# Kernel tuning notes

Hardware: AMD Instinct MI355X
Metric: run time of the kernel (lower is better)

The kernel has to match this reference:

```python
import jax, jax.numpy as jnp
import numpy as np

# --- fake-quant helpers (Brevitas-style simulated int4 with STE) ---

def _fq(x, scale, qmin, qmax):
    # fake quantize with straight-through estimator
    q = jnp.clip(jnp.round(x / scale), qmin, qmax) * scale
    return x + jax.lax.stop_gradient(q - x)

def quant_act_signed4(x):
    # signed 4-bit symmetric activation quant: scale = max|x| / 7
    scale = jax.lax.stop_gradient(jnp.maximum(jnp.max(jnp.abs(x)), 1e-8) / 7.0)
    return _fq(x, scale, -8, 7), scale

def quant_relu4(x):
    # QuantReLU: relu then unsigned 4-bit quant, scale = max / 15
    x = jax.nn.relu(x)
    scale = jax.lax.stop_gradient(jnp.maximum(jnp.max(x), 1e-8) / 15.0)
    return _fq(x, scale, 0, 15), scale

def quant_w4(w):
    # per-tensor symmetric 4-bit weight quant
    scale = jax.lax.stop_gradient(jnp.maximum(jnp.max(jnp.abs(w)), 1e-8) / 7.0)
    return _fq(w, scale, -8, 7), scale

def quant_bias32(b, in_scale, w_scale):
    # Int32Bias: bias quantized at scale = input_scale * weight_scale
    s = in_scale * w_scale
    return _fq(b, s, -(2.0**31), 2.0**31 - 1.0)

def conv2d(x, w, b):
    y = jax.lax.conv_general_dilated(x, w, (1, 1), 'VALID',
                                     dimension_numbers=('NCHW', 'OIHW', 'NCHW'))
    return y + b[None, :, None, None]


def setup_inputs() -> dict:
    key = jax.random.key(0)
    ks = jax.random.split(key, 9)
    f32 = jnp.float32
    return {
        'x':   jax.random.normal(ks[0], (32, 3, 224, 224), f32),
        'w1':  jax.random.normal(ks[1], (32, 3, 3, 3), f32) * 0.1,
        'b1':  jax.random.normal(ks[2], (32,), f32) * 0.05,
        'w2':  jax.random.normal(ks[3], (64, 32, 3, 3), f32) * 0.06,
        'b2':  jax.random.normal(ks[4], (64,), f32) * 0.05,
        'wf1': jax.random.normal(ks[5], (128, 64), f32) * 0.1,
        'bf1': jax.random.normal(ks[6], (128,), f32) * 0.05,
        'wf2': jax.random.normal(ks[7], (10, 128), f32) * 0.08,
        'bf2': jax.random.normal(ks[8], (10,), f32) * 0.05,
    }


def reference(x, w1, b1, w2, b2, wf1, bf1, wf2, bf2):
    # quant_inp
    xq, s_in = quant_act_signed4(x)
    # conv1 (quantized weights, Int32 bias)
    w1q, sw1 = quant_w4(w1)
    y = conv2d(xq, w1q, quant_bias32(b1, s_in, sw1))
    y, s1 = quant_relu4(y)
    # conv2
    w2q, sw2 = quant_w4(w2)
    y = conv2d(y, w2q, quant_bias32(b2, s1, sw2))
    y, s2 = quant_relu4(y)
    # adaptive avg pool to 1x1 + flatten -> [B, 64]
    y = jnp.mean(y, axis=(2, 3))
    # fc1
    wf1q, swf1 = quant_w4(wf1)
    y = y @ wf1q.T + quant_bias32(bf1, s2, swf1)
    y, s3 = quant_relu4(y)
    # fc2
    wf2q, swf2 = quant_w4(wf2)
    y = y @ wf2q.T + quant_bias32(bf2, s3, swf2)
    return jax.nn.log_softmax(y, axis=1)
```

## Files before the change

### kernel.cpp

```cpp
#include <hip/hip_runtime.h>
#include <cstdint>
#include <cstddef>

#define DI __device__ __forceinline__

typedef int v4i  __attribute__((ext_vector_type(4)));
typedef int v16i __attribute__((ext_vector_type(16)));

#if defined(__has_builtin)
#if __has_builtin(__builtin_amdgcn_sdot4)
#define HAS_SDOT4 1
#endif
#if __has_builtin(__builtin_amdgcn_alignbyte)
#define HAS_ALIGNBYTE 1
#endif
#if __has_builtin(__builtin_amdgcn_global_load_lds)
#define HAS_GLLDS 1
#endif
#if __has_builtin(__builtin_amdgcn_perm)
#define HAS_PERM 1
#endif
#endif

DI int dot4(unsigned a, unsigned b, int c) {
#ifdef HAS_SDOT4
  return __builtin_amdgcn_sdot4((int)a, (int)b, c, false);
#else
#pragma unroll
  for (int k = 0; k < 4; ++k)
    c += (int)(signed char)(a >> (8 * k)) * (int)(signed char)(b >> (8 * k));
  return c;
#endif
}

DI unsigned alignb(unsigned hi, unsigned lo, int sh) {
#ifdef HAS_ALIGNBYTE
  return __builtin_amdgcn_alignbyte(hi, lo, sh);
#else
  return sh ? ((lo >> (8 * sh)) | (hi << (32 - 8 * sh))) : lo;
#endif
}

DI unsigned bperm(unsigned hi, unsigned lo, unsigned sel) {
#ifdef HAS_PERM
  return __builtin_amdgcn_perm(hi, lo, sel);
#else
  unsigned r = 0;
#pragma unroll
  for (int i = 0; i < 4; ++i) {
    unsigned s = (sel >> (8 * i)) & 255u;
    unsigned b = (s < 4) ? (lo >> (8 * s)) : (hi >> (8 * (s - 4)));
    r |= (b & 255u) << (8 * i);
  }
  return r;
#endif
}

DI float qclamp(int a, float h) {
  return fminf(fmaxf(rintf((float)a * h), 0.f), 15.f);
}

DI unsigned pack4(float4 v, float s) {
  float f[4] = {v.x, v.y, v.z, v.w};
  unsigned w = 0;
#pragma unroll
  for (int k = 0; k < 4; ++k) {
    float q = rintf(f[k] / s);
    q = fminf(fmaxf(q, -8.f), 7.f);
    w |= ((unsigned)((int)q & 255)) << (8 * k);
  }
  return w;
}

#ifdef HAS_GLLDS
typedef __attribute__((address_space(1))) void glb_void;
typedef __attribute__((address_space(3))) void lds_void;
DI void gl_lds16(const void* g, void* l) {
  __builtin_amdgcn_global_load_lds((const glb_void*)g, (lds_void*)l, 16, 0, 0);
}
#else
DI void gl_lds16(const void* g, void* l) { *(v4i*)l = *(const v4i*)g; }
#endif

struct Scal {
  unsigned max_x, max_w1, max_w2, max_wf1, max_wf2;
  int max1, max2;
};

DI float mkscale(unsigned bits, float d) { return fmaxf(__uint_as_float(bits), 1e-8f) / d; }
DI float d_s_in(const Scal* sc) { return mkscale(sc->max_x, 7.f); }
DI float d_sw1(const Scal* sc)  { return mkscale(sc->max_w1, 7.f); }
DI float d_sw2(const Scal* sc)  { return mkscale(sc->max_w2, 7.f); }
DI float d_s1(const Scal* sc)   { return fmaxf((float)sc->max1 * (d_s_in(sc) * d_sw1(sc)), 1e-8f) / 15.f; }
DI float d_s2(const Scal* sc)   { return fmaxf((float)sc->max2 * (d_s1(sc) * d_sw2(sc)), 1e-8f) / 15.f; }

static constexpr int NX   = 32 * 3 * 224 * 224;
static constexpr int NP1  = 32 * 32 * 222 * 224;
static constexpr int C2_ROWB   = 224 * 32;
static constexpr int C2_HPLANE = 224 * 16;
static constexpr int C2V_BLK   = 1120;
static constexpr int C2V_ROWS  = 22;

DI float wave_maxf(float v) { for (int o = 32; o; o >>= 1) v = fmaxf(v, __shfl_down(v, o, 64)); return v; }
DI int   wave_maxi(int v)   { for (int o = 32; o; o >>= 1) v = max(v, __shfl_down(v, o, 64));   return v; }

DI float block_maxf(float v) {
  __shared__ float s[8];
  v = wave_maxf(v);
  int lane = threadIdx.x & 63, w = threadIdx.x >> 6;
  int nw = (int)(blockDim.x >> 6);
  if (!lane) s[w] = v;
  __syncthreads();
  if (threadIdx.x < 64) {
    float t = ((int)threadIdx.x < nw) ? s[threadIdx.x] : 0.f;
    v = wave_maxf(t);
  }
  return v;
}

DI int block_maxi(int v) {
  __shared__ int s[8];
  v = wave_maxi(v);
  int lane = threadIdx.x & 63, w = threadIdx.x >> 6;
  int nw = (int)(blockDim.x >> 6);
  if (!lane) s[w] = v;
  __syncthreads();
  if (threadIdx.x < 64) {
    int t = ((int)threadIdx.x < nw) ? s[threadIdx.x] : 0;
    v = wave_maxi(t);
  }
  return v;
}

__global__ void k_absmax_xw(const float4* __restrict__ x, int n4,
                            const float* __restrict__ w1, const float* __restrict__ w2,
                            const float* __restrict__ wf1, const float* __restrict__ wf2,
                            Scal* sc) {
  if (blockIdx.x < 1024) {
    float m = 0.f;
    for (int i = blockIdx.x * 256 + threadIdx.x; i < n4; i += 1024 * 256) {
      float4 v = x[i];
      m = fmaxf(m, fmaxf(fmaxf(fabsf(v.x), fabsf(v.y)), fmaxf(fabsf(v.z), fabsf(v.w))));
    }
    m = block_maxf(m);
    if (!threadIdx.x) atomicMax(&sc->max_x, __float_as_uint(m));
    return;
  }
  const float* p; int n; unsigned* slot;
  int wb = blockIdx.x - 1024;
  if (wb == 0)      { p = w1;  n = 864;   slot = &sc->max_w1; }
  else if (wb == 1) { p = w2;  n = 18432; slot = &sc->max_w2; }
  else if (wb == 2) { p = wf1; n = 8192;  slot = &sc->max_wf1; }
  else              { p = wf2; n = 1280;  slot = &sc->max_wf2; }
  float m = 0.f;
  for (int i = threadIdx.x; i < n; i += 256) m = fmaxf(m, fabsf(p[i]));
  m = block_maxf(m);
  if (!threadIdx.x) atomicMax(slot, __float_as_uint(m));
}


DI void kpack0(const unsigned* R, v4i& f) {
  f[0] = (int)bperm(R[1], R[0], 0x04020100u);
  f[1] = (int)bperm(R[2], R[1], 0x05040201u);
  f[2] = (int)bperm(R[3], R[2], 0x06050402u);
  f[3] = (int)bperm(R[5], R[4], 0x04020100u);
}
DI void kpack1(const unsigned* R, v4i& f) {
  f[0] = (int)bperm(R[1], R[0], 0x05040201u);
  f[1] = (int)bperm(R[2], R[1], 0x06050402u);
  f[2] = (int)bperm(0u,   R[3], 0x04020100u);
  f[3] = 0;
}

DI v4i conv1_afrag(const unsigned* lw, int oc, int lhalf) {
  unsigned R[6];
  v4i f;
  if (lhalf == 0) {
#pragma unroll
    for (int s = 0; s < 6; ++s) R[s] = lw[oc * 9 + s];
    kpack0(R, f);
  } else {
#pragma unroll
    for (int s = 0; s < 4; ++s) R[s] = lw[oc * 9 + 5 + s];
    kpack1(R, f);
  }
  return f;
}

DI v4i conv1_bfrag(const signed char* lx, int oh_l, int qb, int sh, int lhalf) {
  unsigned R[6];
  v4i f;
  if (lhalf == 0) {
#pragma unroll
    for (int s = 0; s < 6; ++s) {
      int ic = s / 3, kh = s - ic * 3;
      const signed char* base = lx + (ic * 8 + oh_l + kh) * 224 + qb;
      unsigned d0 = *(const unsigned*)base;
      unsigned d1 = *(const unsigned*)(base + 4);
      R[s] = alignb(d1, d0, sh);
    }
    kpack0(R, f);
  } else {
#pragma unroll
    for (int s = 0; s < 4; ++s) {
      int seg = 5 + s;
      int ic = seg / 3, kh = seg - ic * 3;
      const signed char* base = lx + (ic * 8 + oh_l + kh) * 224 + qb;
      unsigned d0 = *(const unsigned*)base;
      unsigned d1 = *(const unsigned*)(base + 4);
      R[s] = alignb(d1, d0, sh);
    }
    kpack1(R, f);
  }
  return f;
}

DI void conv1_stage(const float4* x, const float* w1, const float* b1,
                    int b, int oh0, int tid, float s_in, float sw1,
                    signed char* lx, unsigned* lw, int* lb) {
  for (int i = tid; i < 288; i += 448) {
    int oc = i / 9, r = i - oc * 9;
    unsigned w = 0;
#pragma unroll
    for (int k = 0; k < 3; ++k) {
      float q = rintf(w1[oc * 27 + r * 3 + k] / sw1);
      q = fminf(fmaxf(q, -8.f), 7.f);
      w |= ((unsigned)((int)q & 255)) << (8 * k);
    }
    lw[i] = w;
  }
  if (tid < 32) lb[tid] = (int)rintf(b1[tid] / (s_in * sw1));
  const float4* src = x + (size_t)b * 3 * 224 * 56;
  unsigned* dst = (unsigned*)lx;
#pragma unroll
  for (int it = 0; it < 3; ++it) {
    int i = it * 448 + tid;
    int row = i / 56, d = i - row * 56;
    int ic = row >> 3, r = row & 7;
    dst[i] = pack4(src[(ic * 224 + (oh0 + r)) * 56 + d], s_in);
  }
}

__global__ void __launch_bounds__(448) k_conv1a(
    const float4* __restrict__ x, const float* __restrict__ w1,
    const float* __restrict__ b1, const float* __restrict__ w2,
    const Scal* __restrict__ sc, unsigned* __restrict__ w2frag,
    int* __restrict__ max1) {
  int tid = threadIdx.x;
  if (blockIdx.x >= 1184) {
    int j = (blockIdx.x - 1184) * 448 + tid;
    if (j < 4608) {
      int icq = j & 7; int t = j >> 3;
      int kw = t % 3; t /= 3;
      int kh = t % 3; int oc = t / 3;
      float s = d_sw2(sc);
      unsigned w = 0;
#pragma unroll
      for (int k = 0; k < 4; ++k) {
        int ic = icq * 4 + k;
        float q = rintf(w2[(oc * 32 + ic) * 9 + kh * 3 + kw] / s);
        q = fminf(fmaxf(q, -8.f), 7.f);
        w |= ((unsigned)((int)q & 255)) << (8 * k);
      }
      int tap = kh * 3 + kw;
      int dl = (oc & 31) | ((icq >> 2) << 5);
      w2frag[(((tap * 2) + (oc >> 5)) * 64 + dl) * 4 + (icq & 3)] = w;
    }
    return;
  }

  __shared__ signed char lx[3 * 8 * 224 + 16];
  __shared__ unsigned lw[288];
  __shared__ int lb[32];
  int strip = blockIdx.x % 37;
  int b = blockIdx.x / 37;
  int oh0 = strip * 6;
  float s_in = d_s_in(sc), sw1 = d_sw1(sc);
  conv1_stage(x, w1, b1, b, oh0, tid, s_in, sw1, lx, lw, lb);
  __syncthreads();

  int lane = tid & 63, wv = tid >> 6;
  int lane31 = lane & 31, lhalf = lane >> 5;
  int p = wv * 32 + lane31;
  int qb = p & ~3, sh = p & 3;
  v4i af = conv1_afrag(lw, lane31, lhalf);
  const v4i* lbv = (const v4i*)lb;
  v4i bq[4];
#pragma unroll
  for (int q = 0; q < 4; ++q) bq[q] = lbv[lhalf + 2 * q];

  int mx = 0;
#pragma unroll
  for (int oh_l = 0; oh_l < 6; ++oh_l) {
    v4i bf = conv1_bfrag(lx, oh_l, qb, sh, lhalf);
    v16i acc;
#pragma unroll
    for (int q = 0; q < 4; ++q)
#pragma unroll
      for (int j = 0; j < 4; ++j) acc[4 * q + j] = bq[q][j];
    acc = __builtin_amdgcn_mfma_i32_32x32x32_i8(af, bf, acc, 0, 0, 0);
    if (p < 222) {
#pragma unroll
      for (int r = 0; r < 16; ++r) mx = max(mx, acc[r]);
    }
  }
  mx = block_maxi(max(mx, 0));
  if (!tid) atomicMax(max1, mx);
}

__global__ void __launch_bounds__(448) k_conv1b(
    const float4* __restrict__ x, const float* __restrict__ w1,
    const float* __restrict__ b1, const Scal* __restrict__ sc,
    unsigned char* __restrict__ y1n) {
  __shared__ signed char lx[3 * 8 * 224 + 16];
  __shared__ unsigned lw[288];
  __shared__ int lb[32];
  int tid = threadIdx.x;
  int strip = blockIdx.x % 37;
  int b = blockIdx.x / 37;
  int oh0 = strip * 6;
  float s_in = d_s_in(sc), sw1 = d_sw1(sc);
  conv1_stage(x, w1, b1, b, oh0, tid, s_in, sw1, lx, lw, lb);
  __syncthreads();

  int lane = tid & 63, wv = tid >> 6;
  int lane31 = lane & 31, lhalf = lane >> 5;
  int p = wv * 32 + lane31;
  int qb = p & ~3, sh = p & 3;
  v4i af = conv1_afrag(lw, lane31, lhalf);
  const v4i* lbv = (const v4i*)lb;
  v4i bq[4];
#pragma unroll
  for (int q = 0; q < 4; ++q) bq[q] = lbv[lhalf + 2 * q];

  float h1 = (s_in * sw1) / d_s1(sc);

#pragma unroll
  for (int oh_l = 0; oh_l < 6; ++oh_l) {
    v4i bf = conv1_bfrag(lx, oh_l, qb, sh, lhalf);
    v16i acc;
#pragma unroll
    for (int q = 0; q < 4; ++q)
#pragma unroll
      for (int j = 0; j < 4; ++j) acc[4 * q + j] = bq[q][j];
    acc = __builtin_amdgcn_mfma_i32_32x32x32_i8(af, bf, acc, 0, 0, 0);
    if (p < 222) {
      size_t rowb = (size_t)(b * 222 + oh0 + oh_l) * C2_ROWB;
      unsigned char* dst0 = y1n + rowb + (size_t)p * 16;
#pragma unroll
      for (int q = 0; q < 4; ++q) {
        int oc0 = 8 * q + 4 * lhalf;
        unsigned cw = 0;
#pragma unroll
        for (int j = 0; j < 4; ++j)
          cw |= ((unsigned)(int)qclamp(acc[4 * q + j], h1)) << (8 * j);
        *(unsigned*)(dst0 + (oc0 >> 4) * C2_HPLANE + (oc0 & 15)) = cw;
      }
    }
  }
}


__global__ void __launch_bounds__(256, 4) k_conv2a(
    const unsigned char* __restrict__ y1n, const unsigned* __restrict__ w2frag,
    const float* __restrict__ b2, const Scal* __restrict__ sc, int* __restrict__ max2) {
  int tid = threadIdx.x;
  int lane = tid & 63, wv = tid >> 6;
  int lane31 = lane & 31, lhalf = lane >> 5;
  int blk = (int)blockIdx.x;
  int blk2 = (blk & 7) * 140 + (blk >> 3);
  int role = blk2 * 4 + wv;
  int img = role / 140;
  int rem = role - img * 140;
  int owg = rem % 7;
  int t7 = rem / 7;
  int hh = t7 & 1;
  int vs = t7 >> 1;
  int j0 = vs * C2V_ROWS;
  int ow0 = owg * 32;

  v4i wb[9];
  const v4i* gW = (const v4i*)w2frag;
#pragma unroll
  for (int t = 0; t < 9; ++t) wb[t] = gW[(t * 2 + hh) * 64 + lane];

  float sb = d_s1(sc) * d_sw2(sc);
  int bias = (int)rintf(b2[hh * 32 + lane31] / sb);

  const unsigned char* base = y1n + (size_t)(img * 222 + j0) * C2_ROWB
                              + (size_t)lhalf * C2_HPLANE
                              + (size_t)(ow0 + lane31) * 16;
  v4i A[4][3];
#pragma unroll
  for (int r = 0; r < 3; ++r)
#pragma unroll
    for (int kw = 0; kw < 3; ++kw)
      A[r][kw] = *(const v4i*)(base + (size_t)r * C2_ROWB + kw * 16);

  int mx = 0;
#pragma unroll
  for (int jj = 0; jj < C2V_ROWS; ++jj) {
    if (jj < C2V_ROWS - 1) {
      const unsigned char* rp = base + (size_t)(jj + 3) * C2_ROWB;
#pragma unroll
      for (int kw = 0; kw < 3; ++kw)
        A[(jj + 3) & 3][kw] = *(const v4i*)(rp + kw * 16);
    }
    v16i acc;
#pragma unroll
    for (int r = 0; r < 16; ++r) acc[r] = bias;
#pragma unroll
    for (int kh = 0; kh < 3; ++kh)
#pragma unroll
      for (int kw = 0; kw < 3; ++kw)
        acc = __builtin_amdgcn_mfma_i32_32x32x32_i8(A[(jj + kh) & 3][kw], wb[kh * 3 + kw], acc, 0, 0, 0);

    if (owg != 6) {
#pragma unroll
      for (int r = 0; r < 16; ++r) mx = max(mx, acc[r]);
    } else {
#pragma unroll
      for (int r = 0; r < 16; ++r) {
        int m = (r & 3) + 8 * (r >> 2) + 4 * lhalf;
        if (ow0 + m < 220) mx = max(mx, acc[r]);
      }
    }
  }
  mx = block_maxi(max(mx, 0));
  if (!tid) atomicMax(max2, mx);
}

__global__ void __launch_bounds__(256, 4) k_conv2b(
    const unsigned char* __restrict__ y1n, const unsigned* __restrict__ w2frag,
    const float* __restrict__ b2, const Scal* __restrict__ sc,
    int* __restrict__ pooled_i) {
  int tid = threadIdx.x;
  int lane = tid & 63, wv = tid >> 6;
  int lane31 = lane & 31, lhalf = lane >> 5;
  int blk = (int)blockIdx.x;
  int blk2 = (blk & 7) * 140 + (blk >> 3);
  int role = blk2 * 4 + wv;
  int img = role / 140;
  int rem = role - img * 140;
  int owg = rem % 7;
  int t7 = rem / 7;
  int hh = t7 & 1;
  int vs = t7 >> 1;
  int j0 = vs * C2V_ROWS;
  int ow0 = owg * 32;

  v4i wb[9];
  const v4i* gW = (const v4i*)w2frag;
#pragma unroll
  for (int t = 0; t < 9; ++t) wb[t] = gW[(t * 2 + hh) * 64 + lane];

  float sb = d_s1(sc) * d_sw2(sc);
  int bias = (int)rintf(b2[hh * 32 + lane31] / sb);
  float h1 = sb * (1.0f / d_s2(sc));

  const unsigned char* base = y1n + (size_t)(img * 222 + j0) * C2_ROWB
                              + (size_t)lhalf * C2_HPLANE
                              + (size_t)(ow0 + lane31) * 16;
  v4i A[4][3];
#pragma unroll
  for (int r = 0; r < 3; ++r)
#pragma unroll
    for (int kw = 0; kw < 3; ++kw)
      A[r][kw] = *(const v4i*)(base + (size_t)r * C2_ROWB + kw * 16);

  float psum = 0.f;
#pragma unroll
  for (int jj = 0; jj < C2V_ROWS; ++jj) {
    if (jj < C2V_ROWS - 1) {
      const unsigned char* rp = base + (size_t)(jj + 3) * C2_ROWB;
#pragma unroll
      for (int kw = 0; kw < 3; ++kw)
        A[(jj + 3) & 3][kw] = *(const v4i*)(rp + kw * 16);
    }
    v16i acc;
#pragma unroll
    for (int r = 0; r < 16; ++r) acc[r] = bias;
#pragma unroll
    for (int kh = 0; kh < 3; ++kh)
#pragma unroll
      for (int kw = 0; kw < 3; ++kw)
        acc = __builtin_amdgcn_mfma_i32_32x32x32_i8(A[(jj + kh) & 3][kw], wb[kh * 3 + kw], acc, 0, 0, 0);

    if (owg != 6) {
#pragma unroll
      for (int r = 0; r < 16; ++r) psum += qclamp(acc[r], h1);
    } else {
#pragma unroll
      for (int r = 0; r < 16; ++r) {
        int m = (r & 3) + 8 * (r >> 2) + 4 * lhalf;
        if (ow0 + m < 220) psum += qclamp(acc[r], h1);
      }
    }
  }
  int s = (int)psum;
  s += __shfl_down(s, 32, 64);
  if (lhalf == 0) atomicAdd(&pooled_i[img * 64 + hh * 32 + lane31], s);
}

__global__ void __launch_bounds__(1024) k_fc(
    const int* __restrict__ pooled_i, const float* __restrict__ wf1,
    const float* __restrict__ bf1, const float* __restrict__ wf2,
    const float* __restrict__ bf2, const Scal* __restrict__ sc,
    float* __restrict__ out) {
  __shared__ float pl[2048];
  __shared__ __align__(16) float wq1[128 * 68];
  __shared__ __align__(16) float y3[32 * 132];
  __shared__ float zz[320];
  __shared__ float s3sh;
  __shared__ float red16[16];
  int tid = threadIdx.x;
  float swf1 = mkscale(sc->max_wf1, 7.f), swf2 = mkscale(sc->max_wf2, 7.f);
  float s2 = d_s2(sc);
  for (int i = tid; i < 2048; i += 1024) pl[i] = (float)pooled_i[i] * s2 / 48400.0f;
  for (int i = tid; i < 8192; i += 1024) {
    float q = rintf(wf1[i] / swf1);
    q = fminf(fmaxf(q, -8.f), 7.f);
    wq1[(i >> 6) * 68 + (i & 63)] = q * swf1;
  }
  __syncthreads();
  float sb1 = s2 * swf1;
  float lmax = 0.f;
#pragma unroll
  for (int o = tid; o < 4096; o += 1024) {
    int b = o >> 7, j = o & 127;
    float acc = rintf(bf1[j] / sb1) * sb1;
    const float4* wr4 = (const float4*)&wq1[j * 68];
    const float4* xr4 = (const float4*)&pl[b * 64];
#pragma unroll
    for (int k4 = 0; k4 < 16; ++k4) {
      float4 w4 = wr4[k4], x4 = xr4[k4];
      acc += x4.x * w4.x + x4.y * w4.y + x4.z * w4.z + x4.w * w4.w;
    }
    float r = fmaxf(acc, 0.f);
    y3[b * 132 + j] = r;
    lmax = fmaxf(lmax, r);
  }
  lmax = wave_maxf(lmax);
  {
    int lane = tid & 63, w = tid >> 6;
    if (!lane) red16[w] = lmax;
  }
  __syncthreads();
  if (tid < 64) {
    float t = (tid < 16) ? red16[tid] : 0.f;
    t = wave_maxf(t);
    if (!tid) s3sh = fmaxf(t, 1e-8f) / 15.f;
  }
  __syncthreads();
  float s3 = s3sh;
  float sb2 = s3 * swf2;
  if (tid < 320) {
    int o = tid;
    int b = o / 10, j = o - b * 10;
    float acc = rintf(bf2[j] / sb2) * sb2;
    const float4* yy4 = (const float4*)&y3[b * 132];
    const float4* wr4 = (const float4*)&wf2[j * 128];
#pragma unroll 8
    for (int k4 = 0; k4 < 32; ++k4) {
      float4 y4 = yy4[k4];
      float4 w4 = wr4[k4];
      float yv[4] = {y4.x, y4.y, y4.z, y4.w};
      float wv4[4] = {w4.x, w4.y, w4.z, w4.w};
#pragma unroll
      for (int e = 0; e < 4; ++e) {
        float q = rintf(yv[e] / s3);
        q = fminf(fmaxf(q, 0.f), 15.f);
        float wv = rintf(wv4[e] / swf2);
        wv = fminf(fmaxf(wv, -8.f), 7.f);
        acc += (q * s3) * (wv * swf2);
      }
    }
    zz[o] = acc;
  }
  __syncthreads();
  if (tid < 32) {
    const float* z = &zz[tid * 10];
    float mm = z[0];
    for (int k = 1; k < 10; ++k) mm = fmaxf(mm, z[k]);
    float ssum = 0.f;
    for (int k = 0; k < 10; ++k) ssum += expf(z[k] - mm);
    float l = mm + logf(ssum);
    for (int k = 0; k < 10; ++k) out[tid * 10 + k] = z[k] - l;
  }
}

extern "C" void kernel_launch(void* const* d_in, const int* in_sizes, int n_in,
                              void* d_out, int out_size, void* d_ws, size_t ws_size,
                              hipStream_t stream) {
  const float* x   = (const float*)d_in[0];
  const float* w1  = (const float*)d_in[1];
  const float* b1  = (const float*)d_in[2];
  const float* w2  = (const float*)d_in[3];
  const float* b2  = (const float*)d_in[4];
  const float* wf1 = (const float*)d_in[5];
  const float* bf1 = (const float*)d_in[6];
  const float* wf2 = (const float*)d_in[7];
  const float* bf2 = (const float*)d_in[8];
  float* out = (float*)d_out;

  char* ws = (char*)d_ws;
  Scal* sc = (Scal*)ws;
  int* pooled_i = (int*)(ws + 1024);
  size_t off = 1024 + 8192;
  unsigned* w2frag = (unsigned*)(ws + off);     off += 4608 * 4;
  off = (off + 255) & ~(size_t)255;
  unsigned char* y1n = (unsigned char*)(ws + off); off += (size_t)NP1 + 256;
  (void)ws_size; (void)in_sizes; (void)n_in; (void)out_size;

  hipMemsetAsync(ws, 0, 1024 + 8192, stream);
  k_absmax_xw<<<1028, 256, 0, stream>>>((const float4*)x, NX / 4, w1, w2, wf1, wf2, sc);
  k_conv1a<<<1184 + 11, 448, 0, stream>>>((const float4*)x, w1, b1, w2, sc, w2frag, &sc->max1);
  k_conv1b<<<1184, 448, 0, stream>>>((const float4*)x, w1, b1, sc, y1n);
  k_conv2a<<<C2V_BLK, 256, 0, stream>>>(y1n, w2frag, b2, sc, &sc->max2);
  k_conv2b<<<C2V_BLK, 256, 0, stream>>>(y1n, w2frag, b2, sc, pooled_i);
  k_fc<<<1, 1024, 0, stream>>>(pooled_i, wf1, bf1, wf2, bf2, sc, out);
}
```

Before: 236.9 us.

## Drop LDS staging in conv1; load and quantize input rows directly in registers

Both conv1 kernels stop staging a quantized 8-row input strip in LDS. Each wave now owns one output-width group and a 6-row vertical strip, and loads its own input columns from global memory. It quantizes them into a rolling register ring of rows and builds the MFMA B fragment without LDS reads or alignbyte shifts. Blocks shrink to 256 threads with XCD-aware block remapping to raise occupancy. The trade-off is that neighbouring lanes and waves reload and requantize overlapping input floats from global memory, using scalar loads instead of coalesced float4 loads.

```diff
diff --git a/kernel.cpp b/kernel.cpp
--- a/kernel.cpp
+++ b/kernel.cpp
@@ -22,17 +22,6 @@
 #endif
 #endif
 
-DI int dot4(unsigned a, unsigned b, int c) {
-#ifdef HAS_SDOT4
-  return __builtin_amdgcn_sdot4((int)a, (int)b, c, false);
-#else
-#pragma unroll
-  for (int k = 0; k < 4; ++k)
-    c += (int)(signed char)(a >> (8 * k)) * (int)(signed char)(b >> (8 * k));
-  return c;
-#endif
-}
-
 DI unsigned alignb(unsigned hi, unsigned lo, int sh) {
 #ifdef HAS_ALIGNBYTE
   return __builtin_amdgcn_alignbyte(hi, lo, sh);
@@ -60,27 +49,16 @@
   return fminf(fmaxf(rintf((float)a * h), 0.f), 15.f);
 }
 
-DI unsigned pack4(float4 v, float s) {
-  float f[4] = {v.x, v.y, v.z, v.w};
+DI unsigned q3(const float* px, float s) {
   unsigned w = 0;
 #pragma unroll
-  for (int k = 0; k < 4; ++k) {
-    float q = rintf(f[k] / s);
+  for (int k = 0; k < 3; ++k) {
+    float q = rintf(px[k] / s);
     q = fminf(fmaxf(q, -8.f), 7.f);
     w |= ((unsigned)((int)q & 255)) << (8 * k);
   }
   return w;
 }
-
-#ifdef HAS_GLLDS
-typedef __attribute__((address_space(1))) void glb_void;
-typedef __attribute__((address_space(3))) void lds_void;
-DI void gl_lds16(const void* g, void* l) {
-  __builtin_amdgcn_global_load_lds((const glb_void*)g, (lds_void*)l, 16, 0, 0);
-}
-#else
-DI void gl_lds16(const void* g, void* l) { *(v4i*)l = *(const v4i*)g; }
-#endif
 
 struct Scal {
   unsigned max_x, max_w1, max_w2, max_wf1, max_wf2;
@@ -100,6 +78,8 @@
 static constexpr int C2_HPLANE = 224 * 16;
 static constexpr int C2V_BLK   = 1120;
 static constexpr int C2V_ROWS  = 22;
+static constexpr int C1V_BLK   = 2072;
+static constexpr int C1V_ROWS  = 6;
 
 DI float wave_maxf(float v) { for (int o = 32; o; o >>= 1) v = fmaxf(v, __shfl_down(v, o, 64)); return v; }
 DI int   wave_maxi(int v)   { for (int o = 32; o; o >>= 1) v = max(v, __shfl_down(v, o, 64));   return v; }
@@ -187,38 +167,9 @@
   return f;
 }
 
-DI v4i conv1_bfrag(const signed char* lx, int oh_l, int qb, int sh, int lhalf) {
-  unsigned R[6];
-  v4i f;
-  if (lhalf == 0) {
-#pragma unroll
-    for (int s = 0; s < 6; ++s) {
-      int ic = s / 3, kh = s - ic * 3;
-      const signed char* base = lx + (ic * 8 + oh_l + kh) * 224 + qb;
-      unsigned d0 = *(const unsigned*)base;
-      unsigned d1 = *(const unsigned*)(base + 4);
-      R[s] = alignb(d1, d0, sh);
-    }
-    kpack0(R, f);
-  } else {
-#pragma unroll
-    for (int s = 0; s < 4; ++s) {
-      int seg = 5 + s;
-      int ic = seg / 3, kh = seg - ic * 3;
-      const signed char* base = lx + (ic * 8 + oh_l + kh) * 224 + qb;
-      unsigned d0 = *(const unsigned*)base;
-      unsigned d1 = *(const unsigned*)(base + 4);
-      R[s] = alignb(d1, d0, sh);
-    }
-    kpack1(R, f);
-  }
-  return f;
-}
-
-DI void conv1_stage(const float4* x, const float* w1, const float* b1,
-                    int b, int oh0, int tid, float s_in, float sw1,
-                    signed char* lx, unsigned* lw, int* lb) {
-  for (int i = tid; i < 288; i += 448) {
+DI void conv1_wstage(const float* w1, const float* b1, int tid,
+                     float s_in, float sw1, unsigned* lw, int* lb) {
+  for (int i = tid; i < 288; i += 256) {
     int oc = i / 9, r = i - oc * 9;
     unsigned w = 0;
 #pragma unroll
@@ -230,25 +181,40 @@
     lw[i] = w;
   }
   if (tid < 32) lb[tid] = (int)rintf(b1[tid] / (s_in * sw1));
-  const float4* src = x + (size_t)b * 3 * 224 * 56;
-  unsigned* dst = (unsigned*)lx;
-#pragma unroll
-  for (int it = 0; it < 3; ++it) {
-    int i = it * 448 + tid;
-    int row = i / 56, d = i - row * 56;
-    int ic = row >> 3, r = row & 7;
-    dst[i] = pack4(src[(ic * 224 + (oh0 + r)) * 56 + d], s_in);
-  }
-}
-
-__global__ void __launch_bounds__(448) k_conv1a(
-    const float4* __restrict__ x, const float* __restrict__ w1,
+}
+
+#define C1_BFRAG(bf, t)                                                    \
+  {                                                                        \
+    unsigned R[6];                                                         \
+    if (lhalf == 0) {                                                      \
+      R[0] = cw[(t) & 3][0]; R[1] = cw[((t) + 1) & 3][0];                  \
+      R[2] = cw[((t) + 2) & 3][0];                                         \
+      R[3] = cw[(t) & 3][1]; R[4] = cw[((t) + 1) & 3][1];                  \
+      R[5] = cw[((t) + 2) & 3][1];                                         \
+      kpack0(R, bf);                                                       \
+    } else {                                                               \
+      R[0] = cw[((t) + 2) & 3][0];                                         \
+      R[1] = cw[(t) & 3][1]; R[2] = cw[((t) + 1) & 3][1];                  \
+      R[3] = cw[((t) + 2) & 3][1];                                         \
+      kpack1(R, bf);                                                       \
+    }                                                                      \
+  }
+
+#define C1_LOAD(bk, rr)                                                    \
+  {                                                                        \
+    const float* r0 = xb + (size_t)(j0 + (rr)) * 224;                      \
+    cw[bk][0] = q3(r0, s_in);                                              \
+    cw[bk][1] = q3(r0 + 224 * 224, s_in);                                  \
+  }
+
+__global__ void __launch_bounds__(256, 4) k_conv1a(
+    const float* __restrict__ x, const float* __restrict__ w1,
     const float* __restrict__ b1, const float* __restrict__ w2,
     const Scal* __restrict__ sc, unsigned* __restrict__ w2frag,
     int* __restrict__ max1) {
   int tid = threadIdx.x;
-  if (blockIdx.x >= 1184) {
-    int j = (blockIdx.x - 1184) * 448 + tid;
+  if (blockIdx.x >= C1V_BLK) {
+    int j = (blockIdx.x - C1V_BLK) * 256 + tid;
     if (j < 4608) {
       int icq = j & 7; int t = j >> 3;
       int kw = t % 3; t /= 3;
@@ -269,30 +235,42 @@
     return;
   }
 
-  __shared__ signed char lx[3 * 8 * 224 + 16];
   __shared__ unsigned lw[288];
   __shared__ int lb[32];
-  int strip = blockIdx.x % 37;
-  int b = blockIdx.x / 37;
-  int oh0 = strip * 6;
   float s_in = d_s_in(sc), sw1 = d_sw1(sc);
-  conv1_stage(x, w1, b1, b, oh0, tid, s_in, sw1, lx, lw, lb);
+  conv1_wstage(w1, b1, tid, s_in, sw1, lw, lb);
   __syncthreads();
 
   int lane = tid & 63, wv = tid >> 6;
   int lane31 = lane & 31, lhalf = lane >> 5;
-  int p = wv * 32 + lane31;
-  int qb = p & ~3, sh = p & 3;
+  int blk = (int)blockIdx.x;
+  int blk2 = (blk & 7) * 259 + (blk >> 3);
+  int role = blk2 * 4 + wv;
+  int img = role / 259;
+  int rem = role - img * 259;
+  int owg = rem % 7, vs = rem / 7;
+  int j0 = vs * C1V_ROWS;
+  int p = owg * 32 + lane31;
+  int pc = (p < 222) ? p : 221;
+
   v4i af = conv1_afrag(lw, lane31, lhalf);
   const v4i* lbv = (const v4i*)lb;
   v4i bq[4];
 #pragma unroll
   for (int q = 0; q < 4; ++q) bq[q] = lbv[lhalf + 2 * q];
 
+  int icA = lhalf ? 1 : 0;
+  const float* xb = x + ((size_t)(img * 3 + icA) * 224) * 224 + pc;
+
+  unsigned cw[4][2];
+  C1_LOAD(0, 0); C1_LOAD(1, 1); C1_LOAD(2, 2);
+
   int mx = 0;
 #pragma unroll
-  for (int oh_l = 0; oh_l < 6; ++oh_l) {
-    v4i bf = conv1_bfrag(lx, oh_l, qb, sh, lhalf);
+  for (int t = 0; t < C1V_ROWS; ++t) {
+    if (t < C1V_ROWS - 1) C1_LOAD((t + 3) & 3, t + 3);
+    v4i bf;
+    C1_BFRAG(bf, t);
     v16i acc;
 #pragma unroll
     for (int q = 0; q < 4; ++q)
@@ -308,25 +286,29 @@
   if (!tid) atomicMax(max1, mx);
 }
 
-__global__ void __launch_bounds__(448) k_conv1b(
-    const float4* __restrict__ x, const float* __restrict__ w1,
+__global__ void __launch_bounds__(256, 4) k_conv1b(
+    const float* __restrict__ x, const float* __restrict__ w1,
     const float* __restrict__ b1, const Scal* __restrict__ sc,
     unsigned char* __restrict__ y1n) {
-  __shared__ signed char lx[3 * 8 * 224 + 16];
   __shared__ unsigned lw[288];
   __shared__ int lb[32];
   int tid = threadIdx.x;
-  int strip = blockIdx.x % 37;
-  int b = blockIdx.x / 37;
-  int oh0 = strip * 6;
   float s_in = d_s_in(sc), sw1 = d_sw1(sc);
-  conv1_stage(x, w1, b1, b, oh0, tid, s_in, sw1, lx, lw, lb);
+  conv1_wstage(w1, b1, tid, s_in, sw1, lw, lb);
   __syncthreads();
 
   int lane = tid & 63, wv = tid >> 6;
   int lane31 = lane & 31, lhalf = lane >> 5;
-  int p = wv * 32 + lane31;
-  int qb = p & ~3, sh = p & 3;
+  int blk = (int)blockIdx.x;
+  int blk2 = (blk & 7) * 259 + (blk >> 3);
+  int role = blk2 * 4 + wv;
+  int img = role / 259;
+  int rem = role - img * 259;
+  int owg = rem % 7, vs = rem / 7;
+  int j0 = vs * C1V_ROWS;
+  int p = owg * 32 + lane31;
+  int pc = (p < 222) ? p : 221;
+
   v4i af = conv1_afrag(lw, lane31, lhalf);
   const v4i* lbv = (const v4i*)lb;
   v4i bq[4];
@@ -334,10 +316,17 @@
   for (int q = 0; q < 4; ++q) bq[q] = lbv[lhalf + 2 * q];
 
   float h1 = (s_in * sw1) / d_s1(sc);
-
-#pragma unroll
-  for (int oh_l = 0; oh_l < 6; ++oh_l) {
-    v4i bf = conv1_bfrag(lx, oh_l, qb, sh, lhalf);
+  int icA = lhalf ? 1 : 0;
+  const float* xb = x + ((size_t)(img * 3 + icA) * 224) * 224 + pc;
+
+  unsigned cw[4][2];
+  C1_LOAD(0, 0); C1_LOAD(1, 1); C1_LOAD(2, 2);
+
+#pragma unroll
+  for (int t = 0; t < C1V_ROWS; ++t) {
+    if (t < C1V_ROWS - 1) C1_LOAD((t + 3) & 3, t + 3);
+    v4i bf;
+    C1_BFRAG(bf, t);
     v16i acc;
 #pragma unroll
     for (int q = 0; q < 4; ++q)
@@ -345,16 +334,16 @@
       for (int j = 0; j < 4; ++j) acc[4 * q + j] = bq[q][j];
     acc = __builtin_amdgcn_mfma_i32_32x32x32_i8(af, bf, acc, 0, 0, 0);
     if (p < 222) {
-      size_t rowb = (size_t)(b * 222 + oh0 + oh_l) * C2_ROWB;
+      size_t rowb = (size_t)(img * 222 + j0 + t) * C2_ROWB;
       unsigned char* dst0 = y1n + rowb + (size_t)p * 16;
 #pragma unroll
       for (int q = 0; q < 4; ++q) {
         int oc0 = 8 * q + 4 * lhalf;
-        unsigned cw = 0;
+        unsigned cwd = 0;
 #pragma unroll
         for (int j = 0; j < 4; ++j)
-          cw |= ((unsigned)(int)qclamp(acc[4 * q + j], h1)) << (8 * j);
-        *(unsigned*)(dst0 + (oc0 >> 4) * C2_HPLANE + (oc0 & 15)) = cw;
+          cwd |= ((unsigned)(int)qclamp(acc[4 * q + j], h1)) << (8 * j);
+        *(unsigned*)(dst0 + (oc0 >> 4) * C2_HPLANE + (oc0 & 15)) = cwd;
       }
     }
   }
@@ -614,8 +603,8 @@
 
   hipMemsetAsync(ws, 0, 1024 + 8192, stream);
   k_absmax_xw<<<1028, 256, 0, stream>>>((const float4*)x, NX / 4, w1, w2, wf1, wf2, sc);
-  k_conv1a<<<1184 + 11, 448, 0, stream>>>((const float4*)x, w1, b1, w2, sc, w2frag, &sc->max1);
-  k_conv1b<<<1184, 448, 0, stream>>>((const float4*)x, w1, b1, sc, y1n);
+  k_conv1a<<<C1V_BLK + 18, 256, 0, stream>>>(x, w1, b1, w2, sc, w2frag, &sc->max1);
+  k_conv1b<<<C1V_BLK, 256, 0, stream>>>(x, w1, b1, sc, y1n);
   k_conv2a<<<C2V_BLK, 256, 0, stream>>>(y1n, w2frag, b2, sc, &sc->max2);
   k_conv2b<<<C2V_BLK, 256, 0, stream>>>(y1n, w2frag, b2, sc, pooled_i);
   k_fc<<<1, 1024, 0, stream>>>(pooled_i, wf1, bf1, wf2, bf2, sc, out);
```

Result: slower. 252.6 us (+6.6%).
